# Performance work log

Hardware: AMD Instinct MI355X
Metric: run time of the kernel (lower is better)

## Reference

```python
import jax, jax.numpy as jnp
import numpy as np

N_E = 1024
E_DIM = 256
BETA = 0.25


def setup_inputs() -> dict:
    key = jax.random.key(0)
    k1, k2 = jax.random.split(key)
    z = jax.random.normal(k1, (16, 256, 64, 64), dtype=jnp.float32)
    # embedding initialized uniform(-1/n_e, 1/n_e)
    emb = jax.random.uniform(k2, (N_E, E_DIM), dtype=jnp.float32,
                             minval=-1.0 / N_E, maxval=1.0 / N_E)
    return {"z": z, "emb": emb}


def reference(z, emb):
    # z: [B, C, H, W] with C == e_dim; emb: [n_e, e_dim]
    z_perm = jnp.transpose(z, (0, 2, 3, 1))            # [B, H, W, C]
    zf = z_perm.reshape(-1, E_DIM)                      # [N, C]

    # pairwise squared distances: ||z||^2 + ||e||^2 - 2 z e^T  -> [N, n_e]
    d = (jnp.sum(zf * zf, axis=1, keepdims=True)
         + jnp.sum(emb * emb, axis=1)
         - 2.0 * jnp.matmul(zf, emb.T))

    idx = jnp.argmin(d, axis=1)                         # [N]
    zq_flat = emb[idx]                                  # gather [N, C]
    z_q = zq_flat.reshape(z_perm.shape)                 # [B, H, W, C]

    one_hot = jax.nn.one_hot(idx, N_E, dtype=jnp.float32)  # [N, n_e]

    codebook_loss = jnp.mean((jax.lax.stop_gradient(z_q) - z_perm) ** 2)
    commitment_loss = jnp.mean((z_q - jax.lax.stop_gradient(z_perm)) ** 2)
    loss = codebook_loss + BETA * commitment_loss

    # straight-through estimator
    z_q = z_perm + jax.lax.stop_gradient(z_q - z_perm)

    e_mean = jnp.mean(one_hot, axis=0)                  # [n_e]
    perplexity = jnp.exp(-jnp.sum(e_mean * jnp.log(e_mean + 1e-10)))

    z_q = jnp.transpose(z_q, (0, 3, 1, 2))              # [B, C, H, W]
    idx_ret = idx[:, None]
    return (z_q, loss, perplexity, one_hot, idx_ret, d)
```

## Files before the change

kernel.cpp:

```cpp
#include <hip/hip_runtime.h>
#include <math.h>


typedef unsigned short ushort;
typedef unsigned int uint;
typedef __attribute__((ext_vector_type(8))) short  bf16x8;
typedef __attribute__((ext_vector_type(8))) ushort ushort8v;
typedef __attribute__((ext_vector_type(4))) float  f32x4;

static const size_t O_LOSS = 16777216;
static const size_t O_PERP = 16777217;
static const size_t O_OH   = 16777218;
static const size_t O_IDX  = 83886082;
static const size_t O_D    = 83951618;

static const size_t WS_ENORM = 0;
static const size_t WS_ZNF   = 4096;
static const size_t WS_IDX   = 266240;
static const size_t WS_HIST  = 528384;
static const size_t WS_FCNT  = 532480;
static const size_t WS_FROWS = 532496;
static const size_t WS_LOSS  = 794640;
static const size_t WS_AHI   = 9191440;
static const size_t WS_BHI   = 42745872;

#define THR_FLAG 4e-4f

__device__ __forceinline__ ushort f2bf(float f) {
  uint u = __float_as_uint(f);
  return (ushort)((u + 0x7FFFu + ((u >> 16) & 1u)) >> 16);
}
__device__ __forceinline__ void gload16(const void* g, void* l) {
  __builtin_amdgcn_global_load_lds(
      (const __attribute__((address_space(1))) void*)g,
      (__attribute__((address_space(3))) void*)l, 16, 0, 0);
}
__device__ __forceinline__ void wavefence() {
  __builtin_amdgcn_sched_barrier(0);
  asm volatile("s_waitcnt lgkmcnt(0)" ::: "memory");
  __builtin_amdgcn_sched_barrier(0);
}

__global__ __launch_bounds__(256) void vq_prep_e(const float* __restrict__ emb,
    float* __restrict__ enormf, ushort* __restrict__ Bhi,
    int* __restrict__ hist, int* __restrict__ flag_cnt) {
  __shared__ double part[256];
  const int t = threadIdx.x;
  const int gid = blockIdx.x * 256 + t;
  const int j = gid >> 2, q = gid & 3;
  if (gid < 1024) hist[gid] = 0;
  if (gid == 0) *flag_cnt = 0;
  const float* e = emb + ((size_t)j << 8) + (q << 6);
  ushort* br = Bhi + ((size_t)j << 8) + (q << 6);
  double s = 0.0;
  for (int k0 = 0; k0 < 64; k0 += 8) {
    const float4 a = *(const float4*)&e[k0];
    const float4 b = *(const float4*)&e[k0 + 4];
    ushort8v v;
    v[0] = f2bf(a.x); v[1] = f2bf(a.y); v[2] = f2bf(a.z); v[3] = f2bf(a.w);
    v[4] = f2bf(b.x); v[5] = f2bf(b.y); v[6] = f2bf(b.z); v[7] = f2bf(b.w);
    *(ushort8v*)&br[k0] = v;
    s += (double)a.x * (double)a.x;  s += (double)a.y * (double)a.y;
    s += (double)a.z * (double)a.z;  s += (double)a.w * (double)a.w;
    s += (double)b.x * (double)b.x;  s += (double)b.y * (double)b.y;
    s += (double)b.z * (double)b.z;  s += (double)b.w * (double)b.w;
  }
  part[t] = s;
  __syncthreads();
  if ((t & 3) == 0)
    enormf[(blockIdx.x << 6) + (t >> 2)] =
        (float)(part[t] + part[t + 1] + part[t + 2] + part[t + 3]);
}

__global__ __launch_bounds__(256) void vq_prep_z(const float* __restrict__ z,
    ushort* __restrict__ Ahi, float* __restrict__ znf) {
  __shared__ float As[256][68];
  __shared__ double znp[64][4];
  const int t = threadIdx.x;
  const int lane = t & 63, quad = t >> 6;
  const int blk = blockIdx.x;
  const float* zb = z + (((size_t)(blk >> 6)) << 20) + (((size_t)(blk & 63)) << 6);
  {
    const int kr = t >> 4, xc = (t & 15) << 2;
    for (int k0 = 0; k0 < 256; k0 += 16) {
      const int k = k0 + kr;
      *(float4*)&As[k][xc] = *(const float4*)&zb[((size_t)k << 12) + xc];
    }
  }
  __syncthreads();
  {
    double s = 0.0;
    const int kb = quad << 6;
    for (int k = 0; k < 64; ++k) { const double v = (double)As[kb + k][lane]; s += v * v; }
    znp[lane][quad] = s;
  }
  __syncthreads();
  const int m0 = ((blk >> 6) << 12) + ((blk & 63) << 6);
  if (t < 64) znf[m0 + t] = (float)(znp[t][0] + znp[t][1] + znp[t][2] + znp[t][3]);
  const int row = t >> 2;
  const int swz = (row & 7) << 3;
  ushort* dst = Ahi + ((size_t)(m0 + row) << 8);
  for (int s = 0; s < 8; ++s) {
    const int k0 = ((t & 3) + (s << 2)) << 3;
    ushort8v v;
#pragma unroll
    for (int i = 0; i < 8; ++i) v[i] = f2bf(As[k0 + i][row]);
    *(ushort8v*)&dst[k0 ^ swz] = v;
  }
}

__global__ __launch_bounds__(512, 4) void vq_mega(const ushort* __restrict__ Ahi,
    const ushort* __restrict__ Bhi, const float* __restrict__ emb,
    const float* __restrict__ znf, const float* __restrict__ enormf,
    float* __restrict__ out, int* __restrict__ idxw, int* __restrict__ hist,
    int* __restrict__ flag_cnt, int* __restrict__ flag_rows,
    double* __restrict__ loss_part) {
  __shared__ ushort As[32768];
  __shared__ ushort Bs[2][4096];

  const int t = threadIdx.x;
  const int lane = t & 63;
  const int w = t >> 6;
  const int wr = w >> 1;
  const int wc = w & 1;
  const int g = lane >> 4, cl = lane & 15;
  const int blk = blockIdx.x;
  const int m0 = blk << 7;
  const int zb = blk >> 5;
  const int r0 = (blk & 31) << 7;
  float* dmat = out + O_D;

  {
    const size_t abase = (size_t)m0 << 8;
    const int off = t << 3;
#pragma unroll
    for (int i = 0; i < 8; ++i)
      gload16(Ahi + abase + (i << 12) + off, &As[(i << 12) + off]);
    gload16(Bhi + ((size_t)(t >> 2) << 8) + ((t & 3) << 3), &Bs[0][t << 3]);
  }

  float zn_[2][4];
#pragma unroll
  for (int ai = 0; ai < 2; ++ai)
#pragma unroll
    for (int rg = 0; rg < 4; ++rg)
      zn_[ai][rg] = znf[m0 + (wr << 5) + (ai << 4) + (g << 2) + rg];

  f32x4 acc[2][4];
#pragma unroll
  for (int a = 0; a < 2; ++a)
#pragma unroll
    for (int b = 0; b < 4; ++b) acc[a][b] = (f32x4)(0.0f);
  float run1[8], run2[8]; int runi[8];
#pragma unroll
  for (int r = 0; r < 8; ++r) { run1[r] = 3.0e38f; run2[r] = 3.0e38f; runi[r] = 0; }

  __syncthreads();

  int cur = 0;
  for (int it = 0; it < 64; ++it) {
    const int nt = it >> 3, kch = it & 7;
    if (it < 63) {
      const int nit = it + 1;
      gload16(Bhi + ((size_t)(nit >> 3) << 15) + ((nit & 7) << 5) +
                  ((size_t)(t >> 2) << 8) + ((t & 3) << 3),
              &Bs[cur ^ 1][t << 3]);
    }
    {
      const int kb = kch << 5;
      bf16x8 av[2], bv[4];
#pragma unroll
      for (int ai = 0; ai < 2; ++ai) {
        const int row = (wr << 5) + (ai << 4) + cl;
        av[ai] = *(const bf16x8*)&As[(row << 8) + ((kb + (g << 3)) ^ ((cl & 7) << 3))];
      }
#pragma unroll
      for (int bj = 0; bj < 4; ++bj)
        bv[bj] = *(const bf16x8*)&Bs[cur][(((wc << 6) + (bj << 4) + cl) << 5) + (g << 3)];
#pragma unroll
      for (int ai = 0; ai < 2; ++ai)
#pragma unroll
        for (int bj = 0; bj < 4; ++bj)
          acc[ai][bj] = __builtin_amdgcn_mfma_f32_16x16x32_bf16(av[ai], bv[bj], acc[ai][bj], 0, 0, 0);
    }
    if (kch == 7) {
      float en_[4];
#pragma unroll
      for (int bj = 0; bj < 4; ++bj)
        en_[bj] = enormf[(nt << 7) + (wc << 6) + (bj << 4) + cl];
#pragma unroll
      for (int ai = 0; ai < 2; ++ai) {
#pragma unroll
        for (int bj = 0; bj < 4; ++bj) {
          const int n = (nt << 7) + (wc << 6) + (bj << 4) + cl;
#pragma unroll
          for (int rg = 0; rg < 4; ++rg) {
            const float S = zn_[ai][rg] + en_[bj];
            const float v = S - 2.0f * acc[ai][bj][rg];
            const int m = m0 + (wr << 5) + (ai << 4) + (g << 2) + rg;
            dmat[((size_t)m << 10) + n] = v;
            const int rr = (ai << 2) + rg;
            if (v < run1[rr]) { run2[rr] = run1[rr]; run1[rr] = v; runi[rr] = n; }
            else if (v < run2[rr]) { run2[rr] = v; }
          }
          acc[ai][bj] = (f32x4)(0.0f);
        }
      }
    }
    __syncthreads();
    cur ^= 1;
  }

  float*  sd1  = (float*)&Bs[0][0];
  int*    si1  = (int*)((char*)&Bs[0][0] + 1024);
  float*  sd2  = (float*)((char*)&Bs[0][0] + 2048);
  int*    idxs = (int*)((char*)&Bs[0][0] + 3072);
  double* red  = (double*)((char*)&Bs[0][0] + 3584);

#pragma unroll
  for (int rr = 0; rr < 8; ++rr) {
    float a1 = run1[rr], a2 = run2[rr]; int ai1 = runi[rr];
    for (int off = 8; off >= 1; off >>= 1) {
      const float o1 = __shfl_xor(a1, off, 16);
      const int   oi = __shfl_xor(ai1, off, 16);
      const float o2 = __shfl_xor(a2, off, 16);
      const float ns = fminf(fminf(a2, o2), fmaxf(a1, o1));
      if (o1 < a1 || (o1 == a1 && oi < ai1)) { a1 = o1; ai1 = oi; }
      a2 = ns;
    }
    if (cl == 0) {
      const int r = (wr << 5) + ((rr >> 2) << 4) + (g << 2) + (rr & 3);
      sd1[(r << 1) + wc] = a1; si1[(r << 1) + wc] = ai1; sd2[(r << 1) + wc] = a2;
    }
  }
  __syncthreads();
  if (t < 128) {
    const float a1 = sd1[t << 1], b1 = sd1[(t << 1) + 1];
    const int ai1 = si1[t << 1], bi1 = si1[(t << 1) + 1];
    const float a2 = sd2[t << 1], b2 = sd2[(t << 1) + 1];
    float d1, d2; int i1;
    if (b1 < a1 || (b1 == a1 && bi1 < ai1)) { d1 = b1; i1 = bi1; d2 = fminf(a1, b2); }
    else { d1 = a1; i1 = ai1; d2 = fminf(b1, a2); }
    const int m = m0 + t;
    idxw[m] = i1; idxs[t] = i1;
    out[O_IDX + m] = (float)i1;
    atomicAdd(&hist[i1], 1);
    if (d2 - d1 < THR_FLAG) {
      const int p = atomicAdd(flag_cnt, 1);
      flag_rows[p] = m;
    }
    red[t] = (double)d1;
  }
  __syncthreads();
  for (int off = 64; off > 0; off >>= 1) {
    if (t < off) red[t] += red[t + off];
    __syncthreads();
  }
  if (t == 0) loss_part[blk] = red[0];
  __syncthreads();

  float2* ohbase = (float2*)(out + O_OH);
  for (int rr = 0; rr < 16; ++rr) {
    const int r = (w << 4) + rr;
    const int idx = idxs[r];
    float2* row = ohbase + (((size_t)(m0 + r)) << 9);
    const int half = idx >> 1;
#pragma unroll
    for (int i = 0; i < 8; ++i) {
      const int slot = (i << 6) + lane;
      float2 v; v.x = 0.0f; v.y = 0.0f;
      if (slot == half) { if (idx & 1) v.y = 1.0f; else v.x = 1.0f; }
      row[slot] = v;
    }
  }

  const int arow = t >> 2, gq = t & 3;
  float* Et = (float*)As;
  for (int ch = 0; ch < 4; ++ch) {
    __syncthreads();
    {
      const int e = idxs[arow];
#pragma unroll
      for (int j2 = 0; j2 < 4; ++j2) {
        const int cb = (gq << 4) + (j2 << 2);
        const float4 ev = *(const float4*)&emb[((size_t)e << 8) + (ch << 6) + cb];
        Et[(cb + 0) * 132 + arow] = ev.x;
        Et[(cb + 1) * 132 + arow] = ev.y;
        Et[(cb + 2) * 132 + arow] = ev.z;
        Et[(cb + 3) * 132 + arow] = ev.w;
      }
    }
    __syncthreads();
#pragma unroll
    for (int i = 0; i < 8; ++i) {
      const int cll = (w << 3) + i;
      const int c = (ch << 6) + cll;
#pragma unroll
      for (int h = 0; h < 2; ++h) {
        const int rr = (h << 6) + lane;
        out[((size_t)zb << 20) + ((size_t)c << 12) + r0 + rr] = Et[cll * 132 + rr];
      }
    }
  }
}

__global__ __launch_bounds__(256) void vq_refine(const float* __restrict__ z,
    const float* __restrict__ emb, const float* __restrict__ znf,
    const float* __restrict__ enormf, const int* __restrict__ flag_cnt,
    const int* __restrict__ flag_rows, int* __restrict__ idxw,
    float* __restrict__ out, int* __restrict__ hist) {
  __shared__ float zbuf[4][256];
  __shared__ int candb[4][256];
  const float* dmat = out + O_D;
  const int t = threadIdx.x;
  const int w = t >> 6, lane = t & 63;
  const int gw = (blockIdx.x << 2) + w;
  const int n = *flag_cnt;
  float* zbw = zbuf[w];
  int* cbw = candb[w];

  for (int f = gw; f < n; f += 4096) {
    const int m = flag_rows[f];
    const float* dr = dmat + ((size_t)m << 10) + (lane << 4);
    float dv[16];
#pragma unroll
    for (int s = 0; s < 8; ++s) {
      const float2 p = *(const float2*)&dr[s << 1];
      dv[2 * s] = p.x; dv[2 * s + 1] = p.y;
    }
    float dmin = dv[0];
#pragma unroll
    for (int s = 1; s < 16; ++s) dmin = fminf(dmin, dv[s]);
#pragma unroll
    for (int off = 1; off < 64; off <<= 1) dmin = fminf(dmin, __shfl_xor(dmin, off));
    const float lim = dmin + THR_FLAG;

    uint hm = 0;
#pragma unroll
    for (int s = 0; s < 16; ++s) if (dv[s] <= lim) hm |= (1u << s);
    const int cnt = __popc(hm);
    int incl = cnt;
#pragma unroll
    for (int off = 1; off < 64; off <<= 1) {
      const int v = __shfl_up(incl, off);
      if (lane >= off) incl += v;
    }
    const int ntot = __shfl(incl, 63);
    int p = incl - cnt;
    for (int s = 0; s < 16; ++s)
      if (hm & (1u << s)) { if (p < 256) cbw[p] = (lane << 4) + s; ++p; }

    const size_t zoff = (((size_t)(m >> 12)) << 20) + (size_t)(m & 4095);
#pragma unroll
    for (int i = 0; i < 4; ++i) {
      const int k = (i << 6) + lane;
      zbw[k] = z[zoff + ((size_t)k << 12)];
    }
    wavefence();

    const float znfm = znf[m];
    const int nc = min(ntot, 256);
    float best = 3.0e38f; int bj = 1 << 30;
    for (int c0 = 0; c0 < nc; c0 += 64) {
      const int ci = c0 + lane;
      float val = 3.0e38f; int iv = 1 << 30;
      if (ci < nc) {
        const int j = cbw[ci];
        const float* er = emb + ((size_t)j << 8);
        float s = 0.0f;
        for (int k = 0; k < 256; ++k) s = fmaf(zbw[k], er[k], s);
        val = (znfm + enormf[j]) - 2.0f * s;
        iv = j;
      }
      if (val < best || (val == best && iv < bj)) { best = val; bj = iv; }
    }
#pragma unroll
    for (int off = 1; off < 64; off <<= 1) {
      const float ov = __shfl_xor(best, off);
      const int oj = __shfl_xor(bj, off);
      if (ov < best || (ov == best && oj < bj)) { best = ov; bj = oj; }
    }

    const int old = idxw[m];
    if (bj != old) {
      if (lane == 0) {
        idxw[m] = bj;
        out[O_IDX + m] = (float)bj;
        out[O_OH + ((size_t)m << 10) + (size_t)old] = 0.0f;
        out[O_OH + ((size_t)m << 10) + (size_t)bj] = 1.0f;
        atomicAdd(&hist[old], -1);
        atomicAdd(&hist[bj], 1);
      }
#pragma unroll
      for (int i = 0; i < 4; ++i) {
        const int k = (i << 6) + lane;
        out[zoff + ((size_t)k << 12)] = emb[((size_t)bj << 8) + k];
      }
    }
    wavefence();
  }
}

__global__ __launch_bounds__(256) void vq_final(const double* __restrict__ loss_part,
    const int* __restrict__ hist, float* __restrict__ out) {
  __shared__ double red[256];
  const int t = threadIdx.x;
  red[t] = loss_part[t] + loss_part[t + 256];
  __syncthreads();
  for (int off = 128; off > 0; off >>= 1) {
    if (t < off) red[t] += red[t + off];
    __syncthreads();
  }
  if (t == 0) out[O_LOSS] = (float)(1.25 * red[0] / 16777216.0);
  __syncthreads();
  double h = 0.0;
  for (int i = t; i < 1024; i += 256) {
    const double p = (double)hist[i] / 65536.0;
    h += p * log(p + 1e-10);
  }
  red[t] = h;
  __syncthreads();
  for (int off = 128; off > 0; off >>= 1) {
    if (t < off) red[t] += red[t + off];
    __syncthreads();
  }
  if (t == 0) out[O_PERP] = (float)exp(-red[0]);
}

extern "C" void kernel_launch(void* const* d_in, const int* in_sizes, int n_in,
                              void* d_out, int out_size, void* d_ws, size_t ws_size,
                              hipStream_t stream) {
  const float* z   = (const float*)d_in[0];
  const float* emb = (const float*)d_in[1];
  float* out = (float*)d_out;
  char* ws = (char*)d_ws;

  float*  enormf    = (float*)(ws + WS_ENORM);
  float*  znf       = (float*)(ws + WS_ZNF);
  int*    idxw      = (int*)(ws + WS_IDX);
  int*    hist      = (int*)(ws + WS_HIST);
  int*    flag_cnt  = (int*)(ws + WS_FCNT);
  int*    flag_rows = (int*)(ws + WS_FROWS);
  double* loss_part = (double*)(ws + WS_LOSS);
  ushort* Ahi       = (ushort*)(ws + WS_AHI);
  ushort* Bhi       = (ushort*)(ws + WS_BHI);

  vq_prep_e<<<16, 256, 0, stream>>>(emb, enormf, Bhi, hist, flag_cnt);
  vq_prep_z<<<1024, 256, 0, stream>>>(z, Ahi, znf);
  vq_mega<<<512, 512, 0, stream>>>(Ahi, Bhi, emb, znf, enormf, out, idxw, hist,
                                   flag_cnt, flag_rows, loss_part);
  vq_refine<<<1024, 256, 0, stream>>>(z, emb, znf, enormf, flag_cnt, flag_rows,
                                      idxw, out, hist);
  vq_final<<<1, 256, 0, stream>>>(loss_part, hist, out);
}
```

Before: 312.4 us.

## Prefetch codebook tiles through registers two steps ahead with lighter barrier

The main GEMM loop now loads codebook B chunks from global memory into registers two iterations in advance and writes them to the double-buffered LDS tile with a plain store. This replaces the direct global-to-LDS loads issued one iteration ahead. The full __syncthreads is swapped for a barrier that only waits on LDS counters, so outstanding global loads are no longer drained each iteration. The refine kernel launch also grows from 1024 to 4096 blocks, which adds parallelism for flagged rows. The register staging adds register pressure, and the buffer-reuse logic relies on careful ordering to avoid LDS races.

```diff
diff --git a/kernel.cpp b/kernel.cpp
--- a/kernel.cpp
+++ b/kernel.cpp
@@ -34,6 +34,13 @@
   __builtin_amdgcn_global_load_lds(
       (const __attribute__((address_space(1))) void*)g,
       (__attribute__((address_space(3))) void*)l, 16, 0, 0);
+}
+__device__ __forceinline__ void lbar() {
+  __builtin_amdgcn_sched_barrier(0);
+  asm volatile("s_waitcnt lgkmcnt(0)" ::: "memory");
+  __builtin_amdgcn_sched_barrier(0);
+  __builtin_amdgcn_s_barrier();
+  __builtin_amdgcn_sched_barrier(0);
 }
 __device__ __forceinline__ void wavefence() {
   __builtin_amdgcn_sched_barrier(0);
@@ -130,14 +137,16 @@
   const int r0 = (blk & 31) << 7;
   float* dmat = out + O_D;
 
+  const size_t bthr = ((size_t)(t >> 2) << 8) + ((t & 3) << 3);
   {
     const size_t abase = (size_t)m0 << 8;
     const int off = t << 3;
 #pragma unroll
     for (int i = 0; i < 8; ++i)
       gload16(Ahi + abase + (i << 12) + off, &As[(i << 12) + off]);
-    gload16(Bhi + ((size_t)(t >> 2) << 8) + ((t & 3) << 3), &Bs[0][t << 3]);
-  }
+  }
+  ushort8v rb0 = *(const ushort8v*)(Bhi + bthr);
+  ushort8v rb1 = *(const ushort8v*)(Bhi + (1 << 5) + bthr);
 
   float zn_[2][4];
 #pragma unroll
@@ -155,60 +164,66 @@
 #pragma unroll
   for (int r = 0; r < 8; ++r) { run1[r] = 3.0e38f; run2[r] = 3.0e38f; runi[r] = 0; }
 
-  __syncthreads();
-
-  int cur = 0;
-  for (int it = 0; it < 64; ++it) {
-    const int nt = it >> 3, kch = it & 7;
-    if (it < 63) {
-      const int nit = it + 1;
-      gload16(Bhi + ((size_t)(nit >> 3) << 15) + ((nit & 7) << 5) +
-                  ((size_t)(t >> 2) << 8) + ((t & 3) << 3),
-              &Bs[cur ^ 1][t << 3]);
-    }
-    {
-      const int kb = kch << 5;
-      bf16x8 av[2], bv[4];
-#pragma unroll
-      for (int ai = 0; ai < 2; ++ai) {
-        const int row = (wr << 5) + (ai << 4) + cl;
-        av[ai] = *(const bf16x8*)&As[(row << 8) + ((kb + (g << 3)) ^ ((cl & 7) << 3))];
-      }
-#pragma unroll
-      for (int bj = 0; bj < 4; ++bj)
-        bv[bj] = *(const bf16x8*)&Bs[cur][(((wc << 6) + (bj << 4) + cl) << 5) + (g << 3)];
-#pragma unroll
-      for (int ai = 0; ai < 2; ++ai)
+  *(ushort8v*)&Bs[0][t << 3] = rb0;
+  __syncthreads();
+
+  for (int nt = 0; nt < 8; ++nt) {
+#pragma unroll
+    for (int kch = 0; kch < 8; ++kch) {
+      const int i = (nt << 3) + kch;
+      if (i < 62) {
+        const int ld = i + 2;
+        const size_t o = ((size_t)(ld >> 3) << 15) + ((size_t)(ld & 7) << 5) + bthr;
+        if (kch & 1) rb1 = *(const ushort8v*)(Bhi + o);
+        else         rb0 = *(const ushort8v*)(Bhi + o);
+      }
+      if (i < 63) {
+        if (kch & 1) *(ushort8v*)&Bs[0][t << 3] = rb0;
+        else         *(ushort8v*)&Bs[1][t << 3] = rb1;
+      }
+      {
+        const int kb = kch << 5;
+        bf16x8 av[2], bv[4];
+#pragma unroll
+        for (int ai = 0; ai < 2; ++ai) {
+          const int row = (wr << 5) + (ai << 4) + cl;
+          av[ai] = *(const bf16x8*)&As[(row << 8) + ((kb + (g << 3)) ^ ((cl & 7) << 3))];
+        }
 #pragma unroll
         for (int bj = 0; bj < 4; ++bj)
-          acc[ai][bj] = __builtin_amdgcn_mfma_f32_16x16x32_bf16(av[ai], bv[bj], acc[ai][bj], 0, 0, 0);
-    }
-    if (kch == 7) {
-      float en_[4];
-#pragma unroll
-      for (int bj = 0; bj < 4; ++bj)
-        en_[bj] = enormf[(nt << 7) + (wc << 6) + (bj << 4) + cl];
-#pragma unroll
-      for (int ai = 0; ai < 2; ++ai) {
-#pragma unroll
-        for (int bj = 0; bj < 4; ++bj) {
-          const int n = (nt << 7) + (wc << 6) + (bj << 4) + cl;
-#pragma unroll
-          for (int rg = 0; rg < 4; ++rg) {
-            const float S = zn_[ai][rg] + en_[bj];
-            const float v = S - 2.0f * acc[ai][bj][rg];
-            const int m = m0 + (wr << 5) + (ai << 4) + (g << 2) + rg;
-            dmat[((size_t)m << 10) + n] = v;
-            const int rr = (ai << 2) + rg;
-            if (v < run1[rr]) { run2[rr] = run1[rr]; run1[rr] = v; runi[rr] = n; }
-            else if (v < run2[rr]) { run2[rr] = v; }
+          bv[bj] = *(const bf16x8*)&Bs[kch & 1][(((wc << 6) + (bj << 4) + cl) << 5) + (g << 3)];
+#pragma unroll
+        for (int ai = 0; ai < 2; ++ai)
+#pragma unroll
+          for (int bj = 0; bj < 4; ++bj)
+            acc[ai][bj] = __builtin_amdgcn_mfma_f32_16x16x32_bf16(av[ai], bv[bj], acc[ai][bj], 0, 0, 0);
+      }
+      if (kch == 7) {
+        float en_[4];
+#pragma unroll
+        for (int bj = 0; bj < 4; ++bj)
+          en_[bj] = enormf[(nt << 7) + (wc << 6) + (bj << 4) + cl];
+#pragma unroll
+        for (int ai = 0; ai < 2; ++ai) {
+#pragma unroll
+          for (int bj = 0; bj < 4; ++bj) {
+            const int n = (nt << 7) + (wc << 6) + (bj << 4) + cl;
+#pragma unroll
+            for (int rg = 0; rg < 4; ++rg) {
+              const float S = zn_[ai][rg] + en_[bj];
+              const float v = S - 2.0f * acc[ai][bj][rg];
+              const int m = m0 + (wr << 5) + (ai << 4) + (g << 2) + rg;
+              dmat[((size_t)m << 10) + n] = v;
+              const int rr = (ai << 2) + rg;
+              if (v < run1[rr]) { run2[rr] = run1[rr]; run1[rr] = v; runi[rr] = n; }
+              else if (v < run2[rr]) { run2[rr] = v; }
+            }
+            acc[ai][bj] = (f32x4)(0.0f);
           }
-          acc[ai][bj] = (f32x4)(0.0f);
         }
       }
-    }
-    __syncthreads();
-    cur ^= 1;
+      lbar();
+    }
   }
 
   float*  sd1  = (float*)&Bs[0][0];
@@ -449,7 +464,7 @@
   vq_prep_z<<<1024, 256, 0, stream>>>(z, Ahi, znf);
   vq_mega<<<512, 512, 0, stream>>>(Ahi, Bhi, emb, znf, enormf, out, idxw, hist,
                                    flag_cnt, flag_rows, loss_part);
-  vq_refine<<<1024, 256, 0, stream>>>(z, emb, znf, enormf, flag_cnt, flag_rows,
+  vq_refine<<<4096, 256, 0, stream>>>(z, emb, znf, enormf, flag_cnt, flag_rows,
                                       idxw, out, hist);
   vq_final<<<1, 256, 0, stream>>>(loss_part, hist, out);
 }
```

New measurement: 331.2 us. +6.0%, slower.

## Halve vq_mega row tile to 64 and regrid warps 2x4 for more blocks

Applied to the files above, without the earlier changes.

Shrinks each vq_mega block from 128 to 64 rows of z, rearranges the 8 waves as 2 row groups by 4 column groups, and doubles the grid to 1024 blocks. The A tile in shared memory halves, and launch bounds now ask for 6 blocks per CU. The argmin merge, loss reduction, one-hot writes and transpose epilogue are reworked for 4 column partials and 64 rows, and vq_final now sums 1024 loss partials. This aims at better occupancy and load balance across CUs, at the cost of loading each codebook tile twice as often and doing less MFMA work per loaded B tile. vq_refine's grid is also raised to 4096 blocks.

```diff
diff --git a/kernel.cpp b/kernel.cpp
--- a/kernel.cpp
+++ b/kernel.cpp
@@ -109,32 +109,32 @@
   }
 }
 
-__global__ __launch_bounds__(512, 4) void vq_mega(const ushort* __restrict__ Ahi,
+__global__ __launch_bounds__(512, 6) void vq_mega(const ushort* __restrict__ Ahi,
     const ushort* __restrict__ Bhi, const float* __restrict__ emb,
     const float* __restrict__ znf, const float* __restrict__ enormf,
     float* __restrict__ out, int* __restrict__ idxw, int* __restrict__ hist,
     int* __restrict__ flag_cnt, int* __restrict__ flag_rows,
     double* __restrict__ loss_part) {
-  __shared__ ushort As[32768];
+  __shared__ ushort As[16384];
   __shared__ ushort Bs[2][4096];
 
   const int t = threadIdx.x;
   const int lane = t & 63;
   const int w = t >> 6;
-  const int wr = w >> 1;
-  const int wc = w & 1;
+  const int wr = w >> 2;
+  const int wc = w & 3;
   const int g = lane >> 4, cl = lane & 15;
   const int blk = blockIdx.x;
-  const int m0 = blk << 7;
-  const int zb = blk >> 5;
-  const int r0 = (blk & 31) << 7;
+  const int m0 = blk << 6;
+  const int zb = blk >> 6;
+  const int r0 = (blk & 63) << 6;
   float* dmat = out + O_D;
 
   {
     const size_t abase = (size_t)m0 << 8;
     const int off = t << 3;
 #pragma unroll
-    for (int i = 0; i < 8; ++i)
+    for (int i = 0; i < 4; ++i)
       gload16(Ahi + abase + (i << 12) + off, &As[(i << 12) + off]);
     gload16(Bhi + ((size_t)(t >> 2) << 8) + ((t & 3) << 3), &Bs[0][t << 3]);
   }
@@ -146,11 +146,11 @@
     for (int rg = 0; rg < 4; ++rg)
       zn_[ai][rg] = znf[m0 + (wr << 5) + (ai << 4) + (g << 2) + rg];
 
-  f32x4 acc[2][4];
+  f32x4 acc[2][2];
 #pragma unroll
   for (int a = 0; a < 2; ++a)
 #pragma unroll
-    for (int b = 0; b < 4; ++b) acc[a][b] = (f32x4)(0.0f);
+    for (int b = 0; b < 2; ++b) acc[a][b] = (f32x4)(0.0f);
   float run1[8], run2[8]; int runi[8];
 #pragma unroll
   for (int r = 0; r < 8; ++r) { run1[r] = 3.0e38f; run2[r] = 3.0e38f; runi[r] = 0; }
@@ -168,31 +168,31 @@
     }
     {
       const int kb = kch << 5;
-      bf16x8 av[2], bv[4];
+      bf16x8 av[2], bv[2];
 #pragma unroll
       for (int ai = 0; ai < 2; ++ai) {
         const int row = (wr << 5) + (ai << 4) + cl;
         av[ai] = *(const bf16x8*)&As[(row << 8) + ((kb + (g << 3)) ^ ((cl & 7) << 3))];
       }
 #pragma unroll
-      for (int bj = 0; bj < 4; ++bj)
-        bv[bj] = *(const bf16x8*)&Bs[cur][(((wc << 6) + (bj << 4) + cl) << 5) + (g << 3)];
+      for (int bj = 0; bj < 2; ++bj)
+        bv[bj] = *(const bf16x8*)&Bs[cur][(((wc << 5) + (bj << 4) + cl) << 5) + (g << 3)];
 #pragma unroll
       for (int ai = 0; ai < 2; ++ai)
 #pragma unroll
-        for (int bj = 0; bj < 4; ++bj)
+        for (int bj = 0; bj < 2; ++bj)
           acc[ai][bj] = __builtin_amdgcn_mfma_f32_16x16x32_bf16(av[ai], bv[bj], acc[ai][bj], 0, 0, 0);
     }
     if (kch == 7) {
-      float en_[4];
-#pragma unroll
-      for (int bj = 0; bj < 4; ++bj)
-        en_[bj] = enormf[(nt << 7) + (wc << 6) + (bj << 4) + cl];
+      float en_[2];
+#pragma unroll
+      for (int bj = 0; bj < 2; ++bj)
+        en_[bj] = enormf[(nt << 7) + (wc << 5) + (bj << 4) + cl];
 #pragma unroll
       for (int ai = 0; ai < 2; ++ai) {
 #pragma unroll
-        for (int bj = 0; bj < 4; ++bj) {
-          const int n = (nt << 7) + (wc << 6) + (bj << 4) + cl;
+        for (int bj = 0; bj < 2; ++bj) {
+          const int n = (nt << 7) + (wc << 5) + (bj << 4) + cl;
 #pragma unroll
           for (int rg = 0; rg < 4; ++rg) {
             const float S = zn_[ai][rg] + en_[bj];
@@ -215,7 +215,7 @@
   int*    si1  = (int*)((char*)&Bs[0][0] + 1024);
   float*  sd2  = (float*)((char*)&Bs[0][0] + 2048);
   int*    idxs = (int*)((char*)&Bs[0][0] + 3072);
-  double* red  = (double*)((char*)&Bs[0][0] + 3584);
+  double* red  = (double*)((char*)&Bs[0][0] + 3328);
 
 #pragma unroll
   for (int rr = 0; rr < 8; ++rr) {
@@ -230,17 +230,19 @@
     }
     if (cl == 0) {
       const int r = (wr << 5) + ((rr >> 2) << 4) + (g << 2) + (rr & 3);
-      sd1[(r << 1) + wc] = a1; si1[(r << 1) + wc] = ai1; sd2[(r << 1) + wc] = a2;
-    }
-  }
-  __syncthreads();
-  if (t < 128) {
-    const float a1 = sd1[t << 1], b1 = sd1[(t << 1) + 1];
-    const int ai1 = si1[t << 1], bi1 = si1[(t << 1) + 1];
-    const float a2 = sd2[t << 1], b2 = sd2[(t << 1) + 1];
-    float d1, d2; int i1;
-    if (b1 < a1 || (b1 == a1 && bi1 < ai1)) { d1 = b1; i1 = bi1; d2 = fminf(a1, b2); }
-    else { d1 = a1; i1 = ai1; d2 = fminf(b1, a2); }
+      sd1[(r << 2) + wc] = a1; si1[(r << 2) + wc] = ai1; sd2[(r << 2) + wc] = a2;
+    }
+  }
+  __syncthreads();
+  if (t < 64) {
+    float d1 = sd1[t << 2]; int i1 = si1[t << 2]; float d2 = sd2[t << 2];
+#pragma unroll
+    for (int e = 1; e < 4; ++e) {
+      const float e1 = sd1[(t << 2) + e]; const int ei = si1[(t << 2) + e];
+      const float e2 = sd2[(t << 2) + e];
+      if (e1 < d1 || (e1 == d1 && ei < i1)) { d2 = fminf(d1, e2); d1 = e1; i1 = ei; }
+      else { d2 = fminf(d2, fminf(e1, e2)); }
+    }
     const int m = m0 + t;
     idxw[m] = i1; idxs[t] = i1;
     out[O_IDX + m] = (float)i1;
@@ -252,7 +254,7 @@
     red[t] = (double)d1;
   }
   __syncthreads();
-  for (int off = 64; off > 0; off >>= 1) {
+  for (int off = 32; off > 0; off >>= 1) {
     if (t < off) red[t] += red[t + off];
     __syncthreads();
   }
@@ -260,8 +262,8 @@
   __syncthreads();
 
   float2* ohbase = (float2*)(out + O_OH);
-  for (int rr = 0; rr < 16; ++rr) {
-    const int r = (w << 4) + rr;
+  for (int rr = 0; rr < 8; ++rr) {
+    const int r = (w << 3) + rr;
     const int idx = idxs[r];
     float2* row = ohbase + (((size_t)(m0 + r)) << 9);
     const int half = idx >> 1;
@@ -274,32 +276,30 @@
     }
   }
 
-  const int arow = t >> 2, gq = t & 3;
+  const int arow = t >> 3, gq = t & 7;
   float* Et = (float*)As;
   for (int ch = 0; ch < 4; ++ch) {
     __syncthreads();
     {
       const int e = idxs[arow];
-#pragma unroll
-      for (int j2 = 0; j2 < 4; ++j2) {
-        const int cb = (gq << 4) + (j2 << 2);
-        const float4 ev = *(const float4*)&emb[((size_t)e << 8) + (ch << 6) + cb];
-        Et[(cb + 0) * 132 + arow] = ev.x;
-        Et[(cb + 1) * 132 + arow] = ev.y;
-        Et[(cb + 2) * 132 + arow] = ev.z;
-        Et[(cb + 3) * 132 + arow] = ev.w;
-      }
+      const int cb = gq << 3;
+      const float4 ev0 = *(const float4*)&emb[((size_t)e << 8) + (ch << 6) + cb];
+      const float4 ev1 = *(const float4*)&emb[((size_t)e << 8) + (ch << 6) + cb + 4];
+      Et[(cb + 0) * 69 + arow] = ev0.x;
+      Et[(cb + 1) * 69 + arow] = ev0.y;
+      Et[(cb + 2) * 69 + arow] = ev0.z;
+      Et[(cb + 3) * 69 + arow] = ev0.w;
+      Et[(cb + 4) * 69 + arow] = ev1.x;
+      Et[(cb + 5) * 69 + arow] = ev1.y;
+      Et[(cb + 6) * 69 + arow] = ev1.z;
+      Et[(cb + 7) * 69 + arow] = ev1.w;
     }
     __syncthreads();
 #pragma unroll
     for (int i = 0; i < 8; ++i) {
       const int cll = (w << 3) + i;
       const int c = (ch << 6) + cll;
-#pragma unroll
-      for (int h = 0; h < 2; ++h) {
-        const int rr = (h << 6) + lane;
-        out[((size_t)zb << 20) + ((size_t)c << 12) + r0 + rr] = Et[cll * 132 + rr];
-      }
+      out[((size_t)zb << 20) + ((size_t)c << 12) + r0 + lane] = Et[cll * 69 + lane];
     }
   }
 }
@@ -405,7 +405,7 @@
     const int* __restrict__ hist, float* __restrict__ out) {
   __shared__ double red[256];
   const int t = threadIdx.x;
-  red[t] = loss_part[t] + loss_part[t + 256];
+  red[t] = loss_part[t] + loss_part[t + 256] + loss_part[t + 512] + loss_part[t + 768];
   __syncthreads();
   for (int off = 128; off > 0; off >>= 1) {
     if (t < off) red[t] += red[t + off];
@@ -447,9 +447,9 @@
 
   vq_prep_e<<<16, 256, 0, stream>>>(emb, enormf, Bhi, hist, flag_cnt);
   vq_prep_z<<<1024, 256, 0, stream>>>(z, Ahi, znf);
-  vq_mega<<<512, 512, 0, stream>>>(Ahi, Bhi, emb, znf, enormf, out, idxw, hist,
-                                   flag_cnt, flag_rows, loss_part);
-  vq_refine<<<1024, 256, 0, stream>>>(z, emb, znf, enormf, flag_cnt, flag_rows,
+  vq_mega<<<1024, 512, 0, stream>>>(Ahi, Bhi, emb, znf, enormf, out, idxw, hist,
+                                    flag_cnt, flag_rows, loss_part);
+  vq_refine<<<4096, 256, 0, stream>>>(z, emb, znf, enormf, flag_cnt, flag_rows,
                                       idxw, out, hist);
   vq_final<<<1, 256, 0, stream>>>(loss_part, hist, out);
 }
```

Measured after the change: 461.7 us. 1.48x slower.
